# Kernel tuning notes

Hardware: AMD Instinct MI355X
Metric: run time of the kernel (lower is better)

The kernel has to match this reference:

```python
import jax, jax.numpy as jnp
import numpy as np

B, T = 64, 512
N_EMB, HIDDEN, VOCAB = 768, 256, 3072


def setup_inputs() -> dict:
    key = jax.random.key(0)
    ks = jax.random.split(key, 5)
    def xavier(k, shape):
        bound = float(np.sqrt(6.0 / (shape[0] + shape[1])))
        return jax.random.uniform(k, shape, jnp.float32, -bound, bound)
    return {
        "idx": jax.random.randint(ks[0], (B, T), 0, VOCAB),
        "emb_table": jax.random.normal(ks[1], (VOCAB, N_EMB), jnp.float32),
        "Wxh": xavier(ks[2], (N_EMB, HIDDEN)),
        "Whh": xavier(ks[3], (HIDDEN, HIDDEN)),
        "Wy": xavier(ks[4], (HIDDEN, VOCAB)),
        "By": jnp.zeros((VOCAB,), jnp.float32),
        "Bh": jnp.zeros((HIDDEN,), jnp.float32),
    }


def reference(idx, emb_table, Wxh, Whh, Wy, By, Bh):
    # embedded: [B, T, E] -> scan over time with hidden carry [B, H]
    embedded = emb_table[idx]                      # gather
    xWxh = jnp.einsum('bte,eh->tbh', embedded, Wxh)  # precompute input projection

    def step(hidden, x_t):
        hidden = jnp.tanh(x_t + hidden @ Whh + Bh)
        return hidden, None

    h0 = jnp.zeros((idx.shape[0], Whh.shape[0]), embedded.dtype)
    hidden, _ = jax.lax.scan(step, h0, xWxh)
    # return_sequences=False: only the last step's output is returned
    out = hidden @ Wy + By
    return out, hidden
```

## Files before the change

kernel.cpp:

```cpp
#include <hip/hip_runtime.h>
#include <hip/hip_bf16.h>

typedef _Float16 half8 __attribute__((ext_vector_type(8)));
typedef float f32x4 __attribute__((ext_vector_type(4)));

#define B_SZ 64
#define T_SZ 512
#define E_SZ 768
#define H_SZ 256
#define V_SZ 3072

#define WS_X     0u
#define WS_WT    16777216u
#define WS_WF    17170432u
#define WS_H     17301504u

static __device__ __forceinline__ float fast_tanh(float x) {
  float e = __builtin_amdgcn_exp2f(x * 2.8853900817779268f);
  return 1.0f - 2.0f * __builtin_amdgcn_rcpf(1.0f + e);
}

__global__ __launch_bounds__(256) void k0_convert(
    const float* __restrict__ Wxh,
    const float* __restrict__ Whh,
    _Float16* __restrict__ Wt,
    _Float16* __restrict__ Wf)
{
  int gid = blockIdx.x * 256 + threadIdx.x;
  if (gid < E_SZ * H_SZ) {
    int e = gid >> 8, h = gid & 255;
    Wt[h * E_SZ + e] = (_Float16)Wxh[gid];
  }
  if (gid < 65536) {
    int j = gid & 7, lane = (gid >> 3) & 63, kt = (gid >> 9) & 7, nt = gid >> 12;
    int quad = lane >> 4, n16 = lane & 15;
    int row = kt * 32 + quad * 8 + j, col = nt * 16 + n16;
    Wf[gid] = (_Float16)Whh[row * H_SZ + col];
  }
}

__global__ __launch_bounds__(256) void k1_xproj(
    const int* __restrict__ idx,
    const float* __restrict__ emb,
    const _Float16* __restrict__ Wt,
    _Float16* __restrict__ x)
{
  const int tid  = threadIdx.x;
  const int w    = tid >> 6;
  const int lane = tid & 63;
  const int m16  = lane & 15;
  const int quad = lane >> 4;
  const int r = blockIdx.x * 64 + w * 16 + m16;
  const int t = r >> 6;
  const int b = r & 63;
  const int erow = idx[b * T_SZ + t];
  const float* Arow = emb + (size_t)erow * E_SZ + quad * 8;

  __shared__ __align__(16) _Float16 bp[2][16 * 64 * 8];
  int n_[4], kb_[4];
#pragma unroll
  for (int pp = 0; pp < 4; ++pp) {
    int f = tid + 256 * pp;
    n_[pp]  = ((f >> 6) << 4) | (f & 15);
    kb_[pp] = (f >> 4) & 3;
  }
  uint4 stg[4];
#pragma unroll
  for (int pp = 0; pp < 4; ++pp)
    stg[pp] = *(const uint4*)(Wt + (size_t)n_[pp] * E_SZ + kb_[pp] * 8);
  f32x4 af0 = *(const f32x4*)(Arow);
  f32x4 af1 = *(const f32x4*)(Arow + 4);

  f32x4 acc[16];
#pragma unroll
  for (int n = 0; n < 16; ++n) { f32x4 z = {0.f, 0.f, 0.f, 0.f}; acc[n] = z; }

#pragma unroll
  for (int pp = 0; pp < 4; ++pp)
    *(uint4*)(bp[0] + (size_t)(tid + 256 * pp) * 8) = stg[pp];
  __syncthreads();

#pragma unroll 1
  for (int ki = 0; ki < 24; ++ki) {
    const _Float16* cur = bp[ki & 1];
    f32x4 af0n = af0, af1n = af1;
    if (ki < 23) {
#pragma unroll
      for (int pp = 0; pp < 4; ++pp)
        stg[pp] = *(const uint4*)(Wt + (size_t)n_[pp] * E_SZ + (ki + 1) * 32 + kb_[pp] * 8);
      af0n = *(const f32x4*)(Arow + (ki + 1) * 32);
      af1n = *(const f32x4*)(Arow + (ki + 1) * 32 + 4);
    }
    half8 a;
#pragma unroll
    for (int e = 0; e < 4; ++e) { a[e] = (_Float16)af0[e]; a[4 + e] = (_Float16)af1[e]; }
#pragma unroll
    for (int nt = 0; nt < 16; ++nt) {
      half8 bb = *(const half8*)(cur + (size_t)(nt * 64 + lane) * 8);
      acc[nt] = __builtin_amdgcn_mfma_f32_16x16x32_f16(a, bb, acc[nt], 0, 0, 0);
    }
    if (ki < 23) {
#pragma unroll
      for (int pp = 0; pp < 4; ++pp)
        *(uint4*)(bp[(ki + 1) & 1] + (size_t)(tid + 256 * pp) * 8) = stg[pp];
      __syncthreads();
    }
    af0 = af0n; af1 = af1n;
  }
  const int rbase = blockIdx.x * 64 + w * 16 + quad * 4;
#pragma unroll
  for (int nt = 0; nt < 16; ++nt) {
    const int col = nt * 16 + m16;
#pragma unroll
    for (int rg = 0; rg < 4; ++rg) {
      x[(size_t)(rbase + rg) * H_SZ + col] = (_Float16)acc[nt][rg];
    }
  }
}

#define LDFRAG(C, KT, R0, R1, R2, R3) { \
  uint4 q = Wf4[(((size_t)(w * 2 + C) * 8 + KT) * 64) + lane]; \
  asm volatile("v_accvgpr_write_b32 a" #R0 ", %0" :: "v"(q.x) : "a" #R0); \
  asm volatile("v_accvgpr_write_b32 a" #R1 ", %0" :: "v"(q.y) : "a" #R1); \
  asm volatile("v_accvgpr_write_b32 a" #R2 ", %0" :: "v"(q.z) : "a" #R2); \
  asm volatile("v_accvgpr_write_b32 a" #R3 ", %0" :: "v"(q.w) : "a" #R3); }

#define MFMA_K0(A0, Z) \
  asm volatile( \
    "v_mfma_f32_16x16x32_f16 %[t0], %[a], a[0:3],   %[z]\n\t" \
    "v_mfma_f32_16x16x32_f16 %[t1], %[a], a[32:35], %[z]" \
    : [t0] "=&v"(acc0), [t1] "=&v"(acc1) \
    : [a] "v"(A0), [z] "v"(Z));

#define MFMA_KT(A0, B0, B1) \
  asm volatile( \
    "v_mfma_f32_16x16x32_f16 %[t0], %[a], a[" #B0 "], %[t0]\n\t" \
    "v_mfma_f32_16x16x32_f16 %[t1], %[a], a[" #B1 "], %[t1]" \
    : [t0] "+v"(acc0), [t1] "+v"(acc1) \
    : [a] "v"(A0));

#define MFMA_K7(A0, B0, B1) \
  asm volatile( \
    "v_mfma_f32_16x16x32_f16 %[t0], %[a], a[" #B0 "], %[t0]\n\t" \
    "v_mfma_f32_16x16x32_f16 %[t1], %[a], a[" #B1 "], %[t1]\n\t" \
    "s_nop 7\n\t" \
    "s_nop 7" \
    : [t0] "+v"(acc0), [t1] "+v"(acc1) \
    : [a] "v"(A0));

__global__ __launch_bounds__(512) void k2_rnn(
    const _Float16* __restrict__ Wf,
    const _Float16* __restrict__ x,
    const float* __restrict__ Bh,
    float* __restrict__ hout,
    float* __restrict__ hidout)
{
  const int b    = blockIdx.x;
  const int tid  = threadIdx.x;
  const int w    = tid >> 6;
  const int lane = tid & 63;
  const int quad = lane >> 4;
  const int n16  = lane & 15;
  __shared__ __align__(16) _Float16 hb[2][H_SZ];
  const uint4* Wf4 = (const uint4*)Wf;

  LDFRAG(0,0,  0,  1,  2,  3)  LDFRAG(0,1,  4,  5,  6,  7)
  LDFRAG(0,2,  8,  9, 10, 11)  LDFRAG(0,3, 12, 13, 14, 15)
  LDFRAG(0,4, 16, 17, 18, 19)  LDFRAG(0,5, 20, 21, 22, 23)
  LDFRAG(0,6, 24, 25, 26, 27)  LDFRAG(0,7, 28, 29, 30, 31)
  LDFRAG(1,0, 32, 33, 34, 35)  LDFRAG(1,1, 36, 37, 38, 39)
  LDFRAG(1,2, 40, 41, 42, 43)  LDFRAG(1,3, 44, 45, 46, 47)
  LDFRAG(1,4, 48, 49, 50, 51)  LDFRAG(1,5, 52, 53, 54, 55)
  LDFRAG(1,6, 56, 57, 58, 59)  LDFRAG(1,7, 60, 61, 62, 63)

  const int col0 = w * 32 + n16;
  const int col1 = col0 + 16;
  const float bh0 = Bh[col0];
  const float bh1 = Bh[col1];
  const _Float16* xp0 = x + b * H_SZ + col0;
  const _Float16* xp1 = x + b * H_SZ + col1;
  _Float16 xq0 = xp0[0], xq1 = xp1[0];
  f32x4 zero4 = {0.f, 0.f, 0.f, 0.f};
  asm volatile("" : "+v"(zero4));
  if (tid < H_SZ) hb[1][tid] = (_Float16)0.f;
  float h0 = 0.f, h1 = 0.f;
  __syncthreads();

#pragma unroll 1
  for (int t = 0; t < T_SZ; ++t) {
    const int tn = (t < T_SZ - 1) ? (t + 1) : t;
    _Float16 xn0 = xp0[(size_t)tn * (B_SZ * H_SZ)];
    _Float16 xn1 = xp1[(size_t)tn * (B_SZ * H_SZ)];
    const _Float16* hr = hb[(t + 1) & 1];
    half8 va0 = *(const half8*)(hr +   0 + quad * 8);
    half8 va1 = *(const half8*)(hr +  32 + quad * 8);
    half8 va2 = *(const half8*)(hr +  64 + quad * 8);
    half8 va3 = *(const half8*)(hr +  96 + quad * 8);
    half8 va4 = *(const half8*)(hr + 128 + quad * 8);
    half8 va5 = *(const half8*)(hr + 160 + quad * 8);
    half8 va6 = *(const half8*)(hr + 192 + quad * 8);
    half8 va7 = *(const half8*)(hr + 224 + quad * 8);
    f32x4 acc0, acc1;
    MFMA_K0(va0, zero4)
    MFMA_KT(va1,  4:7,  36:39)
    MFMA_KT(va2,  8:11, 40:43)
    MFMA_KT(va3, 12:15, 44:47)
    MFMA_KT(va4, 16:19, 48:51)
    MFMA_KT(va5, 20:23, 52:55)
    MFMA_KT(va6, 24:27, 56:59)
    MFMA_K7(va7, 28:31, 60:63)
    h0 = fast_tanh(acc0[0] + (float)xq0 + bh0);
    h1 = fast_tanh(acc1[0] + (float)xq1 + bh1);
    if (quad == 0) {
      hb[t & 1][col0] = (_Float16)h0;
      hb[t & 1][col1] = (_Float16)h1;
    }
    __syncthreads();
    xq0 = xn0; xq1 = xn1;
  }
  if (quad == 0) {
    hout[b * H_SZ + col0] = h0;  hout[b * H_SZ + col1] = h1;
    hidout[b * H_SZ + col0] = h0; hidout[b * H_SZ + col1] = h1;
  }
}

__global__ __launch_bounds__(256) void k3_out(
    const float* __restrict__ h,
    const float* __restrict__ Wy,
    const float* __restrict__ By,
    float* __restrict__ out)
{
  __shared__ float hs[H_SZ];
  const int c = blockIdx.x;
  const int b = blockIdx.y;
  const int v = c * 256 + threadIdx.x;
  hs[threadIdx.x] = h[b * H_SZ + threadIdx.x];
  __syncthreads();
  float acc = By[v];
#pragma unroll 8
  for (int jj = 0; jj < H_SZ; ++jj) {
    acc += hs[jj] * Wy[(size_t)jj * V_SZ + v];
  }
  out[(size_t)b * V_SZ + v] = acc;
}

extern "C" void kernel_launch(void* const* d_in, const int* in_sizes, int n_in,
                              void* d_out, int out_size, void* d_ws, size_t ws_size,
                              hipStream_t stream)
{
  const int*   idx = (const int*)d_in[0];
  const float* emb = (const float*)d_in[1];
  const float* Wxh = (const float*)d_in[2];
  const float* Whh = (const float*)d_in[3];
  const float* Wy  = (const float*)d_in[4];
  const float* By  = (const float*)d_in[5];
  const float* Bh  = (const float*)d_in[6];

  char* ws = (char*)d_ws;
  _Float16* x    = (_Float16*)(ws + WS_X);
  _Float16* Wt   = (_Float16*)(ws + WS_WT);
  _Float16* Wf   = (_Float16*)(ws + WS_WF);
  float*    hbuf = (float*)(ws + WS_H);

  float* out    = (float*)d_out;
  float* hidout = out + (size_t)B_SZ * V_SZ;

  k0_convert<<<768, 256, 0, stream>>>(Wxh, Whh, Wt, Wf);
  k1_xproj  <<<512, 256, 0, stream>>>(idx, emb, Wt, x);
  k2_rnn    <<<64, 512, 0, stream>>>(Wf, x, Bh, hbuf, hidout);
  k3_out    <<<dim3(12, 64), 256, 0, stream>>>(hbuf, Wy, By, out);
}
```

Measured before the change: 387.6 us.

## Split RNN step between MFMA and packed fp16 dot2 VALU paths

In the recurrent kernel, each wave now computes one 16-column tile with a single MFMA chain instead of two. The other 16 columns are computed on the vector ALU using v_dot2 over packed fp16 Whh pairs held in AGPRs, followed by a cross-quad shuffle reduction. The aim is to shorten the serial per-timestep latency by overlapping the MFMA dependency chain with VALU dot products. The cost is extra AGPR reads, extra LDS reads of the hidden state and two shuffles per step, plus a new packed-weight layout built in the convert kernel.

```diff
diff --git a/kernel.cpp b/kernel.cpp
--- a/kernel.cpp
+++ b/kernel.cpp
@@ -2,6 +2,7 @@
 #include <hip/hip_bf16.h>
 
 typedef _Float16 half8 __attribute__((ext_vector_type(8)));
+typedef _Float16 half2t __attribute__((ext_vector_type(2)));
 typedef float f32x4 __attribute__((ext_vector_type(4)));
 
 #define B_SZ 64
@@ -13,7 +14,13 @@
 #define WS_X     0u
 #define WS_WT    16777216u
 #define WS_WF    17170432u
-#define WS_H     17301504u
+#define WS_WP    17301504u
+#define WS_H     17432576u
+
+static __device__ __forceinline__ float dot2p(int hp, unsigned int wp, float c) {
+  return __builtin_amdgcn_fdot2(__builtin_bit_cast(half2t, hp),
+                                __builtin_bit_cast(half2t, wp), c, false);
+}
 
 static __device__ __forceinline__ float fast_tanh(float x) {
   float e = __builtin_amdgcn_exp2f(x * 2.8853900817779268f);
@@ -24,7 +31,8 @@
     const float* __restrict__ Wxh,
     const float* __restrict__ Whh,
     _Float16* __restrict__ Wt,
-    _Float16* __restrict__ Wf)
+    _Float16* __restrict__ Wf,
+    unsigned int* __restrict__ Wp)
 {
   int gid = blockIdx.x * 256 + threadIdx.x;
   if (gid < E_SZ * H_SZ) {
@@ -36,6 +44,14 @@
     int quad = lane >> 4, n16 = lane & 15;
     int row = kt * 32 + quad * 8 + j, col = nt * 16 + n16;
     Wf[gid] = (_Float16)Whh[row * H_SZ + col];
+  }
+  if (gid < 32768) {
+    int j = gid >> 7, k = gid & 127;
+    _Float16 lo = (_Float16)Whh[(2 * k) * H_SZ + j];
+    _Float16 hi = (_Float16)Whh[(2 * k + 1) * H_SZ + j];
+    unsigned short lu = __builtin_bit_cast(unsigned short, lo);
+    unsigned short hu = __builtin_bit_cast(unsigned short, hi);
+    Wp[j * 128 + k] = (unsigned int)lu | ((unsigned int)hu << 16);
   }
 }
 
@@ -118,38 +134,42 @@
   }
 }
 
-#define LDFRAG(C, KT, R0, R1, R2, R3) { \
-  uint4 q = Wf4[(((size_t)(w * 2 + C) * 8 + KT) * 64) + lane]; \
+#define LDFRAG(KT, R0, R1, R2, R3) { \
+  uint4 q = Wf4[(((size_t)(2 * w) * 8 + KT) * 64) + lane]; \
   asm volatile("v_accvgpr_write_b32 a" #R0 ", %0" :: "v"(q.x) : "a" #R0); \
   asm volatile("v_accvgpr_write_b32 a" #R1 ", %0" :: "v"(q.y) : "a" #R1); \
   asm volatile("v_accvgpr_write_b32 a" #R2 ", %0" :: "v"(q.z) : "a" #R2); \
   asm volatile("v_accvgpr_write_b32 a" #R3 ", %0" :: "v"(q.w) : "a" #R3); }
 
-#define MFMA_K0(A0, Z) \
-  asm volatile( \
-    "v_mfma_f32_16x16x32_f16 %[t0], %[a], a[0:3],   %[z]\n\t" \
-    "v_mfma_f32_16x16x32_f16 %[t1], %[a], a[32:35], %[z]" \
-    : [t0] "=&v"(acc0), [t1] "=&v"(acc1) \
-    : [a] "v"(A0), [z] "v"(Z));
-
-#define MFMA_KT(A0, B0, B1) \
-  asm volatile( \
-    "v_mfma_f32_16x16x32_f16 %[t0], %[a], a[" #B0 "], %[t0]\n\t" \
-    "v_mfma_f32_16x16x32_f16 %[t1], %[a], a[" #B1 "], %[t1]" \
-    : [t0] "+v"(acc0), [t1] "+v"(acc1) \
-    : [a] "v"(A0));
-
-#define MFMA_K7(A0, B0, B1) \
-  asm volatile( \
-    "v_mfma_f32_16x16x32_f16 %[t0], %[a], a[" #B0 "], %[t0]\n\t" \
-    "v_mfma_f32_16x16x32_f16 %[t1], %[a], a[" #B1 "], %[t1]\n\t" \
-    "s_nop 7\n\t" \
-    "s_nop 7" \
-    : [t0] "+v"(acc0), [t1] "+v"(acc1) \
-    : [a] "v"(A0));
+#define PARKD(I, R0, R1, R2, R3) { \
+  uint4 p = WpC[I]; \
+  asm volatile("v_accvgpr_write_b32 a" #R0 ", %0" :: "v"(p.x) : "a" #R0); \
+  asm volatile("v_accvgpr_write_b32 a" #R1 ", %0" :: "v"(p.y) : "a" #R1); \
+  asm volatile("v_accvgpr_write_b32 a" #R2 ", %0" :: "v"(p.z) : "a" #R2); \
+  asm volatile("v_accvgpr_write_b32 a" #R3 ", %0" :: "v"(p.w) : "a" #R3); }
+
+#define MFMA_K0(A0) \
+  asm volatile("v_mfma_f32_16x16x32_f16 %[t0], %[a], a[0:3], %[z]" \
+    : [t0] "=&v"(accm) : [a] "v"(A0), [z] "v"(zero4));
+#define MFMA_KT(A0, B) \
+  asm volatile("v_mfma_f32_16x16x32_f16 %[t0], %[a], a[" #B "], %[t0]" \
+    : [t0] "+v"(accm) : [a] "v"(A0));
+#define MFMA_K7(A0, B) \
+  asm volatile("v_mfma_f32_16x16x32_f16 %[t0], %[a], a[" #B "], %[t0]\n\t" \
+    "s_nop 7\n\ts_nop 7" : [t0] "+v"(accm) : [a] "v"(A0));
+
+#define DOT4(HV, R0, R1, R2, R3) { \
+  unsigned w0_, w1_, w2_, w3_; \
+  asm volatile("v_accvgpr_read_b32 %0, a" #R0 : "=v"(w0_)); \
+  asm volatile("v_accvgpr_read_b32 %0, a" #R1 : "=v"(w1_)); \
+  asm volatile("v_accvgpr_read_b32 %0, a" #R2 : "=v"(w2_)); \
+  asm volatile("v_accvgpr_read_b32 %0, a" #R3 : "=v"(w3_)); \
+  s0 = dot2p((int)HV.x, w0_, s0); s1 = dot2p((int)HV.y, w1_, s1); \
+  s2 = dot2p((int)HV.z, w2_, s2); s3 = dot2p((int)HV.w, w3_, s3); }
 
 __global__ __launch_bounds__(512) void k2_rnn(
     const _Float16* __restrict__ Wf,
+    const unsigned int* __restrict__ Wp,
     const _Float16* __restrict__ x,
     const float* __restrict__ Bh,
     float* __restrict__ hout,
@@ -163,22 +183,24 @@
   const int n16  = lane & 15;
   __shared__ __align__(16) _Float16 hb[2][H_SZ];
   const uint4* Wf4 = (const uint4*)Wf;
-
-  LDFRAG(0,0,  0,  1,  2,  3)  LDFRAG(0,1,  4,  5,  6,  7)
-  LDFRAG(0,2,  8,  9, 10, 11)  LDFRAG(0,3, 12, 13, 14, 15)
-  LDFRAG(0,4, 16, 17, 18, 19)  LDFRAG(0,5, 20, 21, 22, 23)
-  LDFRAG(0,6, 24, 25, 26, 27)  LDFRAG(0,7, 28, 29, 30, 31)
-  LDFRAG(1,0, 32, 33, 34, 35)  LDFRAG(1,1, 36, 37, 38, 39)
-  LDFRAG(1,2, 40, 41, 42, 43)  LDFRAG(1,3, 44, 45, 46, 47)
-  LDFRAG(1,4, 48, 49, 50, 51)  LDFRAG(1,5, 52, 53, 54, 55)
-  LDFRAG(1,6, 56, 57, 58, 59)  LDFRAG(1,7, 60, 61, 62, 63)
-
-  const int col0 = w * 32 + n16;
-  const int col1 = col0 + 16;
-  const float bh0 = Bh[col0];
-  const float bh1 = Bh[col1];
-  const _Float16* xp0 = x + b * H_SZ + col0;
-  const _Float16* xp1 = x + b * H_SZ + col1;
+  const uint4* Wp4 = (const uint4*)Wp;
+
+  LDFRAG(0,  0,  1,  2,  3)  LDFRAG(1,  4,  5,  6,  7)
+  LDFRAG(2,  8,  9, 10, 11)  LDFRAG(3, 12, 13, 14, 15)
+  LDFRAG(4, 16, 17, 18, 19)  LDFRAG(5, 20, 21, 22, 23)
+  LDFRAG(6, 24, 25, 26, 27)  LDFRAG(7, 28, 29, 30, 31)
+  const int cd = w * 32 + 16 + n16;
+  const uint4* WpC = Wp4 + ((size_t)cd * 32 + quad * 8);
+  PARKD(0, 32, 33, 34, 35)  PARKD(1, 36, 37, 38, 39)
+  PARKD(2, 40, 41, 42, 43)  PARKD(3, 44, 45, 46, 47)
+  PARKD(4, 48, 49, 50, 51)  PARKD(5, 52, 53, 54, 55)
+  PARKD(6, 56, 57, 58, 59)  PARKD(7, 60, 61, 62, 63)
+
+  const int cm = w * 32 + n16;
+  const float bh0 = Bh[cm];
+  const float bh1 = Bh[cd];
+  const _Float16* xp0 = x + b * H_SZ + cm;
+  const _Float16* xp1 = x + b * H_SZ + cd;
   _Float16 xq0 = xp0[0], xq1 = xp1[0];
   f32x4 zero4 = {0.f, 0.f, 0.f, 0.f};
   asm volatile("" : "+v"(zero4));
@@ -200,27 +222,43 @@
     half8 va5 = *(const half8*)(hr + 160 + quad * 8);
     half8 va6 = *(const half8*)(hr + 192 + quad * 8);
     half8 va7 = *(const half8*)(hr + 224 + quad * 8);
-    f32x4 acc0, acc1;
-    MFMA_K0(va0, zero4)
-    MFMA_KT(va1,  4:7,  36:39)
-    MFMA_KT(va2,  8:11, 40:43)
-    MFMA_KT(va3, 12:15, 44:47)
-    MFMA_KT(va4, 16:19, 48:51)
-    MFMA_KT(va5, 20:23, 52:55)
-    MFMA_KT(va6, 24:27, 56:59)
-    MFMA_K7(va7, 28:31, 60:63)
-    h0 = fast_tanh(acc0[0] + (float)xq0 + bh0);
-    h1 = fast_tanh(acc1[0] + (float)xq1 + bh1);
+    const uint4* hq = (const uint4*)(hr + quad * 64);
+    uint4 hv0 = hq[0], hv1 = hq[1], hv2 = hq[2], hv3 = hq[3];
+    uint4 hv4 = hq[4], hv5 = hq[5], hv6 = hq[6], hv7 = hq[7];
+
+    f32x4 accm;
+    float s0 = 0.f, s1 = 0.f, s2 = 0.f, s3 = 0.f;
+    MFMA_K0(va0)
+    DOT4(hv0, 32, 33, 34, 35)
+    MFMA_KT(va1,  4:7)
+    DOT4(hv1, 36, 37, 38, 39)
+    MFMA_KT(va2,  8:11)
+    DOT4(hv2, 40, 41, 42, 43)
+    MFMA_KT(va3, 12:15)
+    DOT4(hv3, 44, 45, 46, 47)
+    MFMA_KT(va4, 16:19)
+    DOT4(hv4, 48, 49, 50, 51)
+    MFMA_KT(va5, 20:23)
+    DOT4(hv5, 52, 53, 54, 55)
+    MFMA_KT(va6, 24:27)
+    DOT4(hv6, 56, 57, 58, 59)
+    MFMA_K7(va7, 28:31)
+    DOT4(hv7, 60, 61, 62, 63)
+    float yd = (s0 + s1) + (s2 + s3);
+    yd += __shfl_xor(yd, 16, 64);
+    yd += __shfl_xor(yd, 32, 64);
+    h0 = fast_tanh(accm[0] + (float)xq0 + bh0);
+    h1 = fast_tanh(yd + (float)xq1 + bh1);
     if (quad == 0) {
-      hb[t & 1][col0] = (_Float16)h0;
-      hb[t & 1][col1] = (_Float16)h1;
+      hb[t & 1][cm] = (_Float16)h0;
+      hb[t & 1][cd] = (_Float16)h1;
     }
     __syncthreads();
     xq0 = xn0; xq1 = xn1;
   }
   if (quad == 0) {
-    hout[b * H_SZ + col0] = h0;  hout[b * H_SZ + col1] = h1;
-    hidout[b * H_SZ + col0] = h0; hidout[b * H_SZ + col1] = h1;
+    hout[b * H_SZ + cm] = h0;  hout[b * H_SZ + cd] = h1;
+    hidout[b * H_SZ + cm] = h0; hidout[b * H_SZ + cd] = h1;
   }
 }
 
@@ -257,16 +295,17 @@
   const float* Bh  = (const float*)d_in[6];
 
   char* ws = (char*)d_ws;
-  _Float16* x    = (_Float16*)(ws + WS_X);
-  _Float16* Wt   = (_Float16*)(ws + WS_WT);
-  _Float16* Wf   = (_Float16*)(ws + WS_WF);
-  float*    hbuf = (float*)(ws + WS_H);
+  _Float16*     x    = (_Float16*)(ws + WS_X);
+  _Float16*     Wt   = (_Float16*)(ws + WS_WT);
+  _Float16*     Wf   = (_Float16*)(ws + WS_WF);
+  unsigned int* Wp   = (unsigned int*)(ws + WS_WP);
+  float*        hbuf = (float*)(ws + WS_H);
 
   float* out    = (float*)d_out;
   float* hidout = out + (size_t)B_SZ * V_SZ;
 
-  k0_convert<<<768, 256, 0, stream>>>(Wxh, Whh, Wt, Wf);
+  k0_convert<<<768, 256, 0, stream>>>(Wxh, Whh, Wt, Wf, Wp);
   k1_xproj  <<<512, 256, 0, stream>>>(idx, emb, Wt, x);
-  k2_rnn    <<<64, 512, 0, stream>>>(Wf, x, Bh, hbuf, hidout);
+  k2_rnn    <<<64, 512, 0, stream>>>(Wf, Wp, x, Bh, hbuf, hidout);
   k3_out    <<<dim3(12, 64), 256, 0, stream>>>(hbuf, Wy, By, out);
 }
```

After: 572.5 us. 1.48x slower.
